# Kernel optimization log

Hardware: AMD Instinct MI355X
Metric: run time of the kernel (lower is better)

Reference implementation:

```python
import jax, jax.numpy as jnp
import numpy as np

BN_EPS = 1e-5

def conv1x1(x, w, b):
    # x: [N,C,T,V], w: [O,C], b: [O]
    return jnp.einsum('nctv,oc->notv', x, w) + b[None, :, None, None]

def conv9(x, w, b):
    # (9,1) temporal conv, padding (4,0). x: [N,C,T,V], w: [O,C,9], b: [O]
    out = jax.lax.conv_general_dilated(
        x, w[:, :, :, None], window_strides=(1, 1), padding=((4, 4), (0, 0)),
        dimension_numbers=('NCHW', 'OIHW', 'NCHW'))
    return out + b[None, :, None, None]

def attn_adj(f1, f2):
    # f1,f2: [N,inter,T,V] -> softmax over rows (axis -2) of [N,V,V]
    N, ic, T, V = f1.shape
    a1 = jnp.transpose(f1, (0, 3, 1, 2)).reshape(N, V, ic * T)  # permute(0,3,1,2).view
    a2 = f2.reshape(N, ic * T, V)
    scores = jnp.einsum('nvk,nkw->nvw', a1, a2) / (ic * T)
    return jax.nn.softmax(scores, axis=-2)


def setup_inputs() -> dict:
    key = jax.random.key(0)
    ks = jax.random.split(key, 16)
    N, C, T, V, S, IC = 16, 256, 64, 25, 3, 64
    s = lambda k, shape, sc=0.05: jax.random.normal(k, shape, dtype=jnp.float32) * sc
    return {
        'x': jax.random.normal(ks[0], (N, C, T, V), dtype=jnp.float32),
        'A': jax.random.uniform(ks[1], (S, V, V), dtype=jnp.float32),
        'PA': s(ks[2], (S, V, V), 1e-3),
        'wa': s(ks[3], (S, IC, C)), 'ba': jnp.zeros((S, IC), jnp.float32),
        'wb': s(ks[4], (S, IC, C)), 'bb': jnp.zeros((S, IC), jnp.float32),
        'wT1': s(ks[5], (S, IC, C, 9)), 'bT1': jnp.zeros((S, IC), jnp.float32),
        'wT2': s(ks[6], (S, IC, C, 9)), 'bT2': jnp.zeros((S, IC), jnp.float32),
        'wST11': s(ks[7], (S, IC, C, 9)), 'bST11': jnp.zeros((S, IC), jnp.float32),
        'wST12': s(ks[8], (S, IC, C, 9)), 'bST12': jnp.zeros((S, IC), jnp.float32),
        'wd': s(ks[9], (S, C, C)), 'bd': jnp.zeros((S, C), jnp.float32),
        'gamma': jnp.ones((C,), jnp.float32), 'beta': jnp.zeros((C,), jnp.float32),
        'bn_mean': jnp.zeros((C,), jnp.float32), 'bn_var': jnp.ones((C,), jnp.float32),
    }


def reference(x, A, PA, wa, ba, wb, bb, wT1, bT1, wT2, bT2,
              wST11, bST11, wST12, bST12, wd, bd, gamma, beta, bn_mean, bn_var):
    N, C, T, V = x.shape
    I = jnp.eye(V, dtype=x.dtype)
    # Chebyshev-like static graph transforms (computed once in __init__ in torch)
    A_ch4s = jax.nn.softmax((8 * A**4 - 4 * A**2 - 4 * A + I) / V, axis=-2)
    A_ch3 = 4 * A**2 - A - 2 * I
    A_all = A_ch3 + A_ch4s + PA  # [3,V,V]

    xf = x.reshape(N, C * T, V)
    y = 0.0
    for i in range(3):
        A1 = attn_adj(conv1x1(x, wa[i], ba[i]), conv1x1(x, wb[i], bb[i]))
        AT = attn_adj(conv9(x, wT1[i], bT1[i]), conv9(x, wT2[i], bT2[i]))
        # ModuleList append quirk: even i -> 1x1 conv (center tap), odd i -> (9,1) conv
        if i % 2 == 0:
            s1 = conv1x1(x, wST11[i, :, :, 4], bST11[i])
            s2 = conv1x1(x, wST12[i, :, :, 4], bST12[i])
        else:
            s1 = conv9(x, wST11[i], bST11[i])
            s2 = conv9(x, wST12[i], bST12[i])
        AST = attn_adj(s1, s2)
        Ai = A_all[i] + A1 + AT + AST  # [N,V,V]
        z = jnp.einsum('nkv,nvw->nkw', xf, Ai).reshape(N, C, T, V)
        y = y + conv1x1(z, wd[i], bd[i])

    yb = (y - bn_mean[None, :, None, None]) * (gamma[None, :, None, None]
         / jnp.sqrt(bn_var[None, :, None, None] + BN_EPS)) + beta[None, :, None, None]
    return jax.nn.relu(yb + x)  # down is identity (in_channels == out_channels)
```

## Files before the change

### kernel.cpp

```cpp
#include <hip/hip_runtime.h>
#include <hip/hip_bf16.h>

#define NN 16
#define CC 256
#define TT 64
#define VV 25
#define ICC 64
#define TV 1600
#define CTV 409600
#define NICTV 1638400

typedef __bf16 v8bf __attribute__((ext_vector_type(8)));
typedef __bf16 v4bf __attribute__((ext_vector_type(4)));
typedef float f32x16 __attribute__((ext_vector_type(16)));

struct ConvPairs {
  const __bf16* wA[5];
  const __bf16* wB[5];
  const float*  bA[5];
  const float*  bB[5];
};

__global__ __launch_bounds__(256) void prep_k(
    const float* __restrict__ x, __bf16* __restrict__ xt,
    const float* __restrict__ wT1, const float* __restrict__ wT2,
    const float* __restrict__ wST11, const float* __restrict__ wST12,
    __bf16* __restrict__ wT1p, __bf16* __restrict__ wT2p,
    __bf16* __restrict__ wS1p, __bf16* __restrict__ wS2p,
    const float* __restrict__ wa, const float* __restrict__ wb,
    __bf16* __restrict__ wabp, __bf16* __restrict__ wScp,
    const float* __restrict__ wd, __bf16* __restrict__ wdb,
    const float* __restrict__ A, const float* __restrict__ PA,
    float* __restrict__ Aall){
  __shared__ __align__(16) float smf[64*65];
  __bf16* smb = (__bf16*)smf;
  int b = blockIdx.x;
  int tid = threadIdx.x;
  if (b < 64){
    int t = b >> 3, ch = (b >> 1) & 3, o2 = b & 1;
    const float* src; __bf16* dst;
    if (t < 3)      { src = wT1  + (size_t)t*147456;     dst = wT1p + (size_t)t*147456; }
    else if (t < 6) { src = wT2  + (size_t)(t-3)*147456; dst = wT2p + (size_t)(t-3)*147456; }
    else if (t == 6){ src = wST11 + 147456;              dst = wS1p; }
    else            { src = wST12 + 147456;              dst = wS2p; }
    const float* in = src + (size_t)(o2*32)*2304 + ch*576;
    for (int i = tid; i < 32*576; i += 256){
      int row = i / 576, cc = i % 576;
      smb[i] = (__bf16)in[(size_t)row*2304 + cc];
    }
    __syncthreads();
    for (int i = tid; i < 18432; i += 256){
      int e = i & 7, l = (i >> 3) & 63, ks = (i >> 9) & 3, tap = i >> 11;
      int ol = l & 31, hh = l >> 5;
      int cl = ks*16 + hh*8 + e;
      dst[(size_t)((((ch*9 + tap)*4 + ks)*2 + o2)*512) + l*8 + e]
          = smb[ol*576 + cl*9 + tap];
    }
  } else if (b < 74){
    int u = b - 64;
    for (int it = 0; it < 8; ++it){
      int idx = tid + it*256;
      int l = idx & 63, o2 = (idx >> 6) & 1, ks = (idx >> 7) & 7, ch = idx >> 10;
      int o = o2*32 + (l & 31), hh = l >> 5;
      int cb = ch*128 + ks*16 + hh*8;
      __bf16 v[8];
      if (u < 6){
        const float* w = (u < 3) ? (wa + (size_t)u*16384) : (wb + (size_t)(u-3)*16384);
        const float* p = w + (size_t)o*256 + cb;
        #pragma unroll
        for (int e = 0; e < 8; ++e) v[e] = (__bf16)p[e];
      } else {
        int i9 = ((u == 6) || (u == 8)) ? 0 : 2;
        const float* w = ((u < 8) ? wST11 : wST12) + (size_t)i9*147456;
        const float* p = w + ((size_t)o*256 + cb)*9 + 4;
        #pragma unroll
        for (int e = 0; e < 8; ++e) v[e] = (__bf16)p[(size_t)e*9];
      }
      __bf16* dst = (u < 6) ? (wabp + (size_t)u*16384) : (wScp + (size_t)(u-6)*16384);
      #pragma unroll
      for (int e = 0; e < 8; ++e) dst[(size_t)idx*8 + e] = v[e];
    }
  } else if (b < 842){
    int i = (b-74)*256 + tid;
    if (i < 196608) wdb[i] = (__bf16)wd[i];
  } else if (b == 842){
    int t = tid;
    if (t < 75){
      int s = t / 25, w = t % 25;
      float a[25], m[25];
      float mx = -3.4e38f;
      for (int v = 0; v < 25; ++v){
        float av = A[(s*25 + v)*25 + w];
        a[v] = av;
        float d = (v == w) ? 1.f : 0.f;
        float mm = (8.f*av*av*av*av - 4.f*av*av - 4.f*av + d) * 0.04f;
        m[v] = mm;
        mx = fmaxf(mx, mm);
      }
      float sum = 0.f;
      for (int v = 0; v < 25; ++v){ float e = __expf(m[v]-mx); m[v] = e; sum += e; }
      float inv = 1.f/sum;
      for (int v = 0; v < 25; ++v){
        float av = a[v];
        float d = (v == w) ? 1.f : 0.f;
        Aall[(s*25+v)*25 + w] = m[v]*inv + 4.f*av*av - av - 2.f*d + PA[(s*25+v)*25+w];
      }
    }
  } else {
    int idx = b - 843;
    int p0 = (idx % 25)*64, c0 = ((idx/25) & 3)*64, n = idx/100;
    for (int i = tid; i < 4096; i += 256){
      int cc = i >> 6, pp = i & 63;
      smf[cc*65+pp] = x[(size_t)n*CTV + (size_t)(c0+cc)*TV + p0 + pp];
    }
    __syncthreads();
    for (int i = tid; i < 4096; i += 256){
      int pp = i >> 6, cc = i & 63;
      xt[((size_t)n*TV + p0+pp)*256 + c0+cc] = (__bf16)smf[cc*65+pp];
    }
  }
}

template<int NTAPS, int CW>
__global__ __launch_bounds__(256, 2) void conv7_k(const __bf16* __restrict__ xt,
    ConvPairs cp, __bf16* __restrict__ fbuf){
  extern __shared__ __bf16 sm[];
  constexpr int HALO  = (NTAPS==9) ? 100 : 0;
  constexpr int NROWS = 256 + 2*HALO;
  constexpr int GPR   = CW/8;
  constexpr int NCH   = 256/CW;
  constexpr int KS    = CW/16;
  constexpr int NSTEP = NTAPS*KS;
  int p0 = blockIdx.x*256;
  int n  = blockIdx.y;
  int pr = blockIdx.z;
  int tid = threadIdx.x;
  int lane = tid & 63;
  int wq = tid >> 6;
  int h = lane >> 5, l31 = lane & 31;
  const __bf16* wpA = cp.wA[pr] + lane*8;
  const __bf16* wpB = cp.wB[pr] + lane*8;
  const __bf16* xtn = xt + (size_t)n*CTV;

  f32x16 acc[4][2];
  #pragma unroll
  for (int a=0;a<4;++a)
    #pragma unroll
    for (int b=0;b<2;++b)
      #pragma unroll
      for (int r=0;r<16;++r) acc[a][b][r] = 0.f;

  int rowbase = wq*64 + l31;

  for (int ch=0; ch<NCH; ++ch){
    for (int s2 = tid; s2 < NROWS*GPR; s2 += 256){
      int row = s2 / GPR, g = s2 % GPR;
      int pg = p0 - HALO + row;
      uint4 val = make_uint4(0u,0u,0u,0u);
      if ((unsigned)pg < 1600u)
        val = *(const uint4*)(xtn + (size_t)pg*256 + ch*CW + g*8);
      int gs = (g + row) & (GPR-1);
      *(uint4*)(sm + row*CW + gs*8) = val;
    }
    __syncthreads();
    auto ldA = [&](int s, v8bf* aa){
      int tap = s / KS, ks = s % KS;
      size_t o = (size_t)((ch*NTAPS + tap)*KS + ks)*1024;
      aa[0] = *(const v8bf*)(wpA + o);
      aa[1] = *(const v8bf*)(wpA + o + 512);
      aa[2] = *(const v8bf*)(wpB + o);
      aa[3] = *(const v8bf*)(wpB + o + 512);
    };
    auto ldB = [&](int s, v8bf* bb){
      int tap = s / KS, ks = s % KS;
      int rowb = (NTAPS==9 ? tap*25 : 0) + rowbase;
      #pragma unroll
      for (int pq=0; pq<2; ++pq){
        int row = rowb + pq*32;
        int gs = ((ks*2 + h) + row) & (GPR-1);
        bb[pq] = *(const v8bf*)(sm + row*CW + gs*8);
      }
    };
    v8bf ar[2][4];
    ldA(0, ar[0]);
    ldA(1, ar[1]);
    v8bf bc[2], bn[2];
    ldB(0, bc);
    #pragma unroll
    for (int s=0; s<NSTEP; ++s){
      if (s+1 < NSTEP) ldB(s+1, bn);
      int cur = s & 1;
      v8bf A0 = ar[cur][0], A1 = ar[cur][1], A2 = ar[cur][2], A3 = ar[cur][3];
      if (s+2 < NSTEP) ldA(s+2, ar[cur]);
      #pragma unroll
      for (int pq=0; pq<2; ++pq){
        acc[0][pq] = __builtin_amdgcn_mfma_f32_32x32x16_bf16(A0, bc[pq], acc[0][pq], 0,0,0);
        acc[1][pq] = __builtin_amdgcn_mfma_f32_32x32x16_bf16(A1, bc[pq], acc[1][pq], 0,0,0);
        acc[2][pq] = __builtin_amdgcn_mfma_f32_32x32x16_bf16(A2, bc[pq], acc[2][pq], 0,0,0);
        acc[3][pq] = __builtin_amdgcn_mfma_f32_32x32x16_bf16(A3, bc[pq], acc[3][pq], 0,0,0);
      }
      bc[0] = bn[0]; bc[1] = bn[1];
    }
    __syncthreads();
  }

  #pragma unroll
  for (int f=0; f<4; ++f){
    int which = f >> 1, o2 = f & 1;
    const float* bias = which ? cp.bB[pr] : cp.bA[pr];
    __bf16* outb = fbuf + (size_t)(pr*2 + which)*NICTV + (size_t)n*TV*64;
    #pragma unroll
    for (int pq=0; pq<2; ++pq){
      int p = p0 + wq*64 + pq*32 + l31;
      if (p >= 1600) continue;
      __bf16* orow = outb + (size_t)p*64;
      #pragma unroll
      for (int g=0; g<4; ++g){
        int og = o2*32 + 8*g + 4*h;
        v4bf pk;
        #pragma unroll
        for (int j=0;j<4;++j) pk[j] = (__bf16)(acc[f][pq][4*g+j] + bias[og+j]);
        *(v4bf*)(orow + og) = pk;
      }
    }
  }
}

__global__ __launch_bounds__(256, 2) void ugemm5_k(const __bf16* __restrict__ xt,
    const __bf16* __restrict__ wdb, __bf16* __restrict__ ubuf){
  extern __shared__ __bf16 sm[];
  int p0 = blockIdx.x*128;
  int n  = blockIdx.y;
  int br = blockIdx.z;
  int tid = threadIdx.x;
  int lane = tid & 63;
  int os = tid >> 6;
  int h = lane >> 5, l31 = lane & 31;
  const __bf16* xtn = xt + (size_t)n*CTV;

  f32x16 acc[2][4];
  #pragma unroll
  for (int a=0;a<2;++a)
    #pragma unroll
    for (int b=0;b<4;++b)
      #pragma unroll
      for (int r=0;r<16;++r) acc[a][b][r] = 0.f;

  for (int s2 = tid; s2 < 128*32; s2 += 256){
    int row = s2 >> 5, g = s2 & 31;
    int pg = p0 + row;
    uint4 val = make_uint4(0u,0u,0u,0u);
    if (pg < 1600)
      val = *(const uint4*)(xtn + (size_t)pg*256 + g*8);
    int gs = (g + row) & 31;
    *(uint4*)(sm + row*256 + gs*8) = val;
  }
  __syncthreads();

  const __bf16* wl = wdb + ((size_t)br*256 + os*64 + l31)*256 + h*8;
  auto ldA = [&](int ks, v8bf& A0, v8bf& A1){
    A0 = *(const v8bf*)(wl + ks*16);
    A1 = *(const v8bf*)(wl + (size_t)32*256 + ks*16);
  };
  auto ldB = [&](int ks, v8bf* bb){
    #pragma unroll
    for (int pq=0; pq<4; ++pq){
      int row = pq*32 + l31;
      int gs = ((ks*2 + h) + row) & 31;
      bb[pq] = *(const v8bf*)(sm + row*256 + gs*8);
    }
  };
  v8bf a0[4], a1[4];
  ldA(0, a0[0], a1[0]);
  ldA(1, a0[1], a1[1]);
  ldA(2, a0[2], a1[2]);
  ldA(3, a0[3], a1[3]);
  v8bf bc[4], bn[4];
  ldB(0, bc);
  #pragma unroll
  for (int ks=0; ks<16; ++ks){
    if (ks+1 < 16) ldB(ks+1, bn);
    int cur = ks & 3;
    v8bf A0 = a0[cur], A1 = a1[cur];
    if (ks+4 < 16) ldA(ks+4, a0[cur], a1[cur]);
    #pragma unroll
    for (int pq=0; pq<4; ++pq){
      acc[0][pq] = __builtin_amdgcn_mfma_f32_32x32x16_bf16(A0, bc[pq], acc[0][pq], 0,0,0);
      acc[1][pq] = __builtin_amdgcn_mfma_f32_32x32x16_bf16(A1, bc[pq], acc[1][pq], 0,0,0);
    }
    #pragma unroll
    for (int pq=0; pq<4; ++pq) bc[pq] = bn[pq];
  }

  #pragma unroll
  for (int pq=0; pq<4; ++pq){
    int p = p0 + pq*32 + l31;
    if (p >= 1600) continue;
    __bf16* out = ubuf + ((size_t)(br*NN + n)*TV + p)*256;
    #pragma unroll
    for (int oq=0; oq<2; ++oq){
      #pragma unroll
      for (int g=0; g<4; ++g){
        int og = os*64 + oq*32 + 8*g + 4*h;
        v4bf pk;
        #pragma unroll
        for (int j=0;j<4;++j) pk[j] = (__bf16)acc[oq][pq][4*g+j];
        *(v4bf*)(out + og) = pk;
      }
    }
  }
}

__global__ __launch_bounds__(256) void scores_m_k(const __bf16* __restrict__ fbuf,
                                                  float* __restrict__ part, int pairbase){
  int n = blockIdx.y, pr = blockIdx.z;
  int tid = threadIdx.x;
  int lane = tid & 63;
  int wave = tid >> 6;
  int chunk = blockIdx.x*4 + wave;
  int h = lane >> 5, l31 = lane & 31;
  const __bf16* f1 = fbuf + (size_t)(pr*2)*NICTV   + (size_t)n*TV*64;
  const __bf16* f2 = fbuf + (size_t)(pr*2+1)*NICTV + (size_t)n*TV*64;
  int t0 = chunk*4;

  f32x16 acc;
  #pragma unroll
  for (int r=0;r<16;++r) acc[r] = 0.f;

  auto off = [&](int s)->size_t{
    int t = t0 + (s>>2), og = s&3;
    return ((size_t)(t*25 + l31))*64 + og*16 + h*8;
  };
  v8bf A[2], B[2];
  { size_t o0 = off(0); A[0] = *(const v8bf*)(f1+o0); B[0] = *(const v8bf*)(f2+o0); }
  { size_t o1 = off(1); A[1] = *(const v8bf*)(f1+o1); B[1] = *(const v8bf*)(f2+o1); }
  #pragma unroll
  for (int s=0; s<16; ++s){
    int cur = s & 1;
    v8bf Ac = A[cur], Bc = B[cur];
    if (s+2 < 16){
      size_t o2 = off(s+2);
      A[cur] = *(const v8bf*)(f1+o2);
      B[cur] = *(const v8bf*)(f2+o2);
    }
    acc = __builtin_amdgcn_mfma_f32_32x32x16_bf16(Ac, Bc, acc, 0,0,0);
  }

  size_t tile = (((size_t)(pairbase+pr)*NN + n)*16 + chunk);
  float* pt = part + tile*1024;
  #pragma unroll
  for (int r=0; r<16; ++r){
    int row = (r&3) + 8*(r>>2) + 4*h;
    pt[row*32 + l31] = acc[r];
  }
}

__global__ __launch_bounds__(64) void reduce_all_k(const float* __restrict__ part,
    const float* __restrict__ Aall, float* __restrict__ Ai3){
  const int pairbr[9] = {0,1,2,0,2, 0,1,2,1};
  int n = blockIdx.x, w = blockIdx.y;
  int lane = threadIdx.x;
  float accbr[3] = {0.f, 0.f, 0.f};
  for (int pr=0; pr<9; ++pr){
    float s = 0.f;
    if (lane < 25){
      const float* pp = part + (((size_t)pr*NN + n)*16)*1024 + lane*32 + w;
      #pragma unroll
      for (int ch=0; ch<16; ++ch) s += pp[(size_t)ch*1024];
    }
    s *= (1.f/4096.f);
    float mval = (lane<25) ? s : -3.4e38f;
    #pragma unroll
    for (int d=32; d>0; d>>=1) mval = fmaxf(mval, __shfl_xor(mval, d));
    float e = (lane<25) ? __expf(s - mval) : 0.f;
    float sum = e;
    #pragma unroll
    for (int d=32; d>0; d>>=1) sum += __shfl_xor(sum, d);
    accbr[pairbr[pr]] += e / sum;
  }
  if (lane < 25){
    #pragma unroll
    for (int br=0; br<3; ++br)
      Ai3[((size_t)br*NN + n)*625 + lane*25 + w] =
        Aall[br*625 + lane*25 + w] + accbr[br];
  }
}

__global__ __launch_bounds__(256) void yep_k(const float* __restrict__ x,
    const float* __restrict__ Ai3, const __bf16* __restrict__ ubuf,
    const float* __restrict__ bd, const float* __restrict__ gamma,
    const float* __restrict__ beta, const float* __restrict__ bnm,
    const float* __restrict__ bnv, float* __restrict__ out){
  __shared__ float ais[3][25*28];
  int t = blockIdx.x, n = blockIdx.y, o = threadIdx.x;
  for (int l=o; l<2100; l+=256){
    int br = l/700, r = l%700;
    int v = r/28, w = r%28;
    ais[br][v*28+w] = (w<25) ? Ai3[((size_t)br*NN + n)*625 + v*25 + w] : 0.f;
  }
  __syncthreads();
  float y[28];
  #pragma unroll
  for (int w=0;w<28;++w) y[w]=0.f;
  for (int br=0; br<3; ++br){
    const __bf16* up = ubuf + ((size_t)(br*NN + n)*TV + t*25)*256 + o;
    float uv[25];
    #pragma unroll
    for (int v=0;v<25;++v) uv[v] = (float)up[(size_t)v*256];
    const float* ab = ais[br];
    for (int v=0; v<25; ++v){
      float u = uv[v];
      #pragma unroll
      for (int j=0; j<7; ++j){
        float4 a4 = *(const float4*)(ab + v*28 + 4*j);
        y[4*j+0] = fmaf(u, a4.x, y[4*j+0]);
        y[4*j+1] = fmaf(u, a4.y, y[4*j+1]);
        y[4*j+2] = fmaf(u, a4.z, y[4*j+2]);
        y[4*j+3] = fmaf(u, a4.w, y[4*j+3]);
      }
    }
  }
  float bsum = bd[o] + bd[256+o] + bd[512+o];
  float sc = gamma[o] * rsqrtf(bnv[o] + 1e-5f);
  float m  = bnm[o], be = beta[o];
  const float* xr = x + (size_t)n*CTV + (size_t)o*TV + t*25;
  float* orow = out + (size_t)n*CTV + (size_t)o*TV + t*25;
  #pragma unroll
  for (int w=0; w<25; ++w)
    orow[w] = fmaxf((y[w] + bsum - m)*sc + be + xr[w], 0.f);
}

extern "C" void kernel_launch(void* const* d_in, const int* in_sizes, int n_in,
                              void* d_out, int out_size, void* d_ws, size_t ws_size,
                              hipStream_t stream) {
  const float* x     = (const float*)d_in[0];
  const float* A     = (const float*)d_in[1];
  const float* PA    = (const float*)d_in[2];
  const float* wa    = (const float*)d_in[3];
  const float* ba    = (const float*)d_in[4];
  const float* wb    = (const float*)d_in[5];
  const float* bb    = (const float*)d_in[6];
  const float* wT1   = (const float*)d_in[7];
  const float* bT1   = (const float*)d_in[8];
  const float* wT2   = (const float*)d_in[9];
  const float* bT2   = (const float*)d_in[10];
  const float* wST11 = (const float*)d_in[11];
  const float* bST11 = (const float*)d_in[12];
  const float* wST12 = (const float*)d_in[13];
  const float* bST12 = (const float*)d_in[14];
  const float* wd    = (const float*)d_in[15];
  const float* bd    = (const float*)d_in[16];
  const float* gamma = (const float*)d_in[17];
  const float* beta  = (const float*)d_in[18];
  const float* bnm   = (const float*)d_in[19];
  const float* bnv   = (const float*)d_in[20];

  char* W = (char*)d_ws;
  float*  Aall = (float*)W;  W += 8192;
  float*  Ai3  = (float*)W;  W += 122880;
  __bf16* wabp = (__bf16*)W; W += 196608;
  __bf16* wScp = (__bf16*)W; W += 131072;
  __bf16* wT1p = (__bf16*)W; W += 884736;
  __bf16* wT2p = (__bf16*)W; W += 884736;
  __bf16* wS1p = (__bf16*)W; W += 294912;
  __bf16* wS2p = (__bf16*)W; W += 294912;
  __bf16* wdb  = (__bf16*)W; W += 393216;
  __bf16* xt   = (__bf16*)W; W += 13107200;
  char* R = W;               W += 39321600;
  float*  part = (float*)W;  W += 9437184;
  __bf16* fbuf = (__bf16*)R;
  __bf16* ubuf = (__bf16*)R;

  prep_k<<<2443, 256, 0, stream>>>(x, xt, wT1, wT2, wST11, wST12,
                                   wT1p, wT2p, wS1p, wS2p,
                                   wa, wb, wabp, wScp, wd, wdb, A, PA, Aall);

  {
    ConvPairs cp;
    for (int i=0;i<3;++i){
      cp.wA[i] = wabp + (size_t)i*16384;      cp.wB[i] = wabp + (size_t)(3+i)*16384;
      cp.bA[i] = ba + i*64;                   cp.bB[i] = bb + i*64;
    }
    int evens[2] = {0, 2};
    for (int j=0;j<2;++j){
      int i = evens[j];
      cp.wA[3+j] = wScp + (size_t)j*16384;    cp.wB[3+j] = wScp + (size_t)(2+j)*16384;
      cp.bA[3+j] = bST11 + i*64;              cp.bB[3+j] = bST12 + i*64;
    }
    conv7_k<1,128><<<dim3(7,16,5), 256, 256*128*2, stream>>>(xt, cp, fbuf);
    scores_m_k<<<dim3(4,16,5), 256, 0, stream>>>(fbuf, part, 0);
  }

  {
    ConvPairs cp;
    for (int i=0;i<3;++i){
      cp.wA[i] = wT1p + (size_t)i*147456;  cp.wB[i] = wT2p + (size_t)i*147456;
      cp.bA[i] = bT1 + i*64;               cp.bB[i] = bT2 + i*64;
    }
    cp.wA[3] = wS1p;  cp.wB[3] = wS2p;
    cp.bA[3] = bST11 + 64;  cp.bB[3] = bST12 + 64;
    cp.wA[4] = cp.wA[3]; cp.wB[4] = cp.wB[3]; cp.bA[4] = cp.bA[3]; cp.bB[4] = cp.bB[3];
    conv7_k<9,64><<<dim3(7,16,4), 256, 456*64*2, stream>>>(xt, cp, fbuf);
    scores_m_k<<<dim3(4,16,4), 256, 0, stream>>>(fbuf, part, 5);
  }

  ugemm5_k<<<dim3(13,16,3), 256, 128*256*2, stream>>>(xt, wdb, ubuf);
  reduce_all_k<<<dim3(16,25), 64, 0, stream>>>(part, Aall, Ai3);
  yep_k<<<dim3(64,16), 256, 0, stream>>>(x, Ai3, ubuf, bd, gamma, beta, bnm, bnv,
                                         (float*)d_out);
}
```

Measured before the change: 357.0 us.

## Double the conv block to 512 threads and prefetch the next channel chunk into registers

The conv kernel now runs 512 threads per block, each wave owning 32 positions instead of 64, which halves the accumulators per thread and targets higher occupancy (launch bounds 512,4). It issues global loads for the next channel chunk into registers while the current chunk's MFMAs run, then writes them to shared memory between barriers, so staging overlaps with compute. Weight and shared-memory fragment prefetch depth rises to four steps. The ugemm and scores kernels likewise get deeper register prefetch. The cost is more live registers per thread and an extra barrier per chunk.

```diff
diff --git a/kernel.cpp b/kernel.cpp
--- a/kernel.cpp
+++ b/kernel.cpp
@@ -122,7 +122,7 @@
 }
 
 template<int NTAPS, int CW>
-__global__ __launch_bounds__(256, 2) void conv7_k(const __bf16* __restrict__ xt,
+__global__ __launch_bounds__(512, 4) void conv8_k(const __bf16* __restrict__ xt,
     ConvPairs cp, __bf16* __restrict__ fbuf){
   extern __shared__ __bf16 sm[];
   constexpr int HALO  = (NTAPS==9) ? 100 : 0;
@@ -131,6 +131,8 @@
   constexpr int NCH   = 256/CW;
   constexpr int KS    = CW/16;
   constexpr int NSTEP = NTAPS*KS;
+  constexpr int NSL   = NROWS*GPR;
+  constexpr int NLD   = (NSL + 511)/512;
   int p0 = blockIdx.x*256;
   int n  = blockIdx.y;
   int pr = blockIdx.z;
@@ -142,84 +144,105 @@
   const __bf16* wpB = cp.wB[pr] + lane*8;
   const __bf16* xtn = xt + (size_t)n*CTV;
 
-  f32x16 acc[4][2];
+  f32x16 acc[4];
   #pragma unroll
   for (int a=0;a<4;++a)
     #pragma unroll
-    for (int b=0;b<2;++b)
-      #pragma unroll
-      for (int r=0;r<16;++r) acc[a][b][r] = 0.f;
-
-  int rowbase = wq*64 + l31;
+    for (int r=0;r<16;++r) acc[a][r] = 0.f;
+
+  int rowbase = wq*32 + l31;
+
+  uint4 sv[NLD];
+  auto stageIssue = [&](int ch){
+    #pragma unroll
+    for (int k=0; k<NLD; ++k){
+      int s2 = tid + k*512;
+      uint4 val = make_uint4(0u,0u,0u,0u);
+      if ((NSL % 512 == 0) || (s2 < NSL)){
+        int row = s2 / GPR, g = s2 % GPR;
+        int pg = p0 - HALO + row;
+        if ((unsigned)pg < 1600u)
+          val = *(const uint4*)(xtn + (size_t)pg*256 + ch*CW + g*8);
+      }
+      sv[k] = val;
+    }
+  };
+  auto stageWrite = [&](){
+    #pragma unroll
+    for (int k=0; k<NLD; ++k){
+      int s2 = tid + k*512;
+      if ((NSL % 512 == 0) || (s2 < NSL)){
+        int row = s2 / GPR, g = s2 % GPR;
+        int gs = (g + row) & (GPR-1);
+        *(uint4*)(sm + row*CW + gs*8) = sv[k];
+      }
+    }
+  };
+
+  auto ldA = [&](int ch, int s, v8bf* aa){
+    int tap = s / KS, ks = s % KS;
+    size_t o = (size_t)((ch*NTAPS + tap)*KS + ks)*1024;
+    aa[0] = *(const v8bf*)(wpA + o);
+    aa[1] = *(const v8bf*)(wpA + o + 512);
+    aa[2] = *(const v8bf*)(wpB + o);
+    aa[3] = *(const v8bf*)(wpB + o + 512);
+  };
+  auto ldB = [&](int s, v8bf& bb){
+    int tap = s / KS, ks = s % KS;
+    int row = (NTAPS==9 ? tap*25 : 0) + rowbase;
+    int gs = ((ks*2 + h) + row) & (GPR-1);
+    bb = *(const v8bf*)(sm + row*CW + gs*8);
+  };
+
+  v8bf ar[4][4];
+  v8bf br_[4];
+
+  #pragma unroll
+  for (int s=0;s<4;++s) ldA(0, s, ar[s]);
+  stageIssue(0);
+  stageWrite();
+  __syncthreads();
 
   for (int ch=0; ch<NCH; ++ch){
-    for (int s2 = tid; s2 < NROWS*GPR; s2 += 256){
-      int row = s2 / GPR, g = s2 % GPR;
-      int pg = p0 - HALO + row;
-      uint4 val = make_uint4(0u,0u,0u,0u);
-      if ((unsigned)pg < 1600u)
-        val = *(const uint4*)(xtn + (size_t)pg*256 + ch*CW + g*8);
-      int gs = (g + row) & (GPR-1);
-      *(uint4*)(sm + row*CW + gs*8) = val;
-    }
-    __syncthreads();
-    auto ldA = [&](int s, v8bf* aa){
-      int tap = s / KS, ks = s % KS;
-      size_t o = (size_t)((ch*NTAPS + tap)*KS + ks)*1024;
-      aa[0] = *(const v8bf*)(wpA + o);
-      aa[1] = *(const v8bf*)(wpA + o + 512);
-      aa[2] = *(const v8bf*)(wpB + o);
-      aa[3] = *(const v8bf*)(wpB + o + 512);
-    };
-    auto ldB = [&](int s, v8bf* bb){
-      int tap = s / KS, ks = s % KS;
-      int rowb = (NTAPS==9 ? tap*25 : 0) + rowbase;
-      #pragma unroll
-      for (int pq=0; pq<2; ++pq){
-        int row = rowb + pq*32;
-        int gs = ((ks*2 + h) + row) & (GPR-1);
-        bb[pq] = *(const v8bf*)(sm + row*CW + gs*8);
-      }
-    };
-    v8bf ar[2][4];
-    ldA(0, ar[0]);
-    ldA(1, ar[1]);
-    v8bf bc[2], bn[2];
-    ldB(0, bc);
+    if (ch+1 < NCH) stageIssue(ch+1);
+    ldB(0, br_[0]); ldB(1, br_[1]); ldB(2, br_[2]); ldB(3, br_[3]);
     #pragma unroll
     for (int s=0; s<NSTEP; ++s){
-      if (s+1 < NSTEP) ldB(s+1, bn);
-      int cur = s & 1;
-      v8bf A0 = ar[cur][0], A1 = ar[cur][1], A2 = ar[cur][2], A3 = ar[cur][3];
-      if (s+2 < NSTEP) ldA(s+2, ar[cur]);
-      #pragma unroll
-      for (int pq=0; pq<2; ++pq){
-        acc[0][pq] = __builtin_amdgcn_mfma_f32_32x32x16_bf16(A0, bc[pq], acc[0][pq], 0,0,0);
-        acc[1][pq] = __builtin_amdgcn_mfma_f32_32x32x16_bf16(A1, bc[pq], acc[1][pq], 0,0,0);
-        acc[2][pq] = __builtin_amdgcn_mfma_f32_32x32x16_bf16(A2, bc[pq], acc[2][pq], 0,0,0);
-        acc[3][pq] = __builtin_amdgcn_mfma_f32_32x32x16_bf16(A3, bc[pq], acc[3][pq], 0,0,0);
-      }
-      bc[0] = bn[0]; bc[1] = bn[1];
-    }
-    __syncthreads();
-  }
-
-  #pragma unroll
-  for (int f=0; f<4; ++f){
-    int which = f >> 1, o2 = f & 1;
-    const float* bias = which ? cp.bB[pr] : cp.bA[pr];
-    __bf16* outb = fbuf + (size_t)(pr*2 + which)*NICTV + (size_t)n*TV*64;
-    #pragma unroll
-    for (int pq=0; pq<2; ++pq){
-      int p = p0 + wq*64 + pq*32 + l31;
-      if (p >= 1600) continue;
-      __bf16* orow = outb + (size_t)p*64;
+      int c = s & 3;
+      v8bf B0 = br_[c];
+      v8bf A0 = ar[c][0], A1 = ar[c][1], A2 = ar[c][2], A3 = ar[c][3];
+      if (s+4 < NSTEP){
+        ldB(s+4, br_[c]);
+        ldA(ch, s+4, ar[c]);
+      } else if (ch+1 < NCH){
+        ldA(ch+1, s+4-NSTEP, ar[c]);
+      }
+      acc[0] = __builtin_amdgcn_mfma_f32_32x32x16_bf16(A0, B0, acc[0], 0,0,0);
+      acc[1] = __builtin_amdgcn_mfma_f32_32x32x16_bf16(A1, B0, acc[1], 0,0,0);
+      acc[2] = __builtin_amdgcn_mfma_f32_32x32x16_bf16(A2, B0, acc[2], 0,0,0);
+      acc[3] = __builtin_amdgcn_mfma_f32_32x32x16_bf16(A3, B0, acc[3], 0,0,0);
+    }
+    if (ch+1 < NCH){
+      __syncthreads();
+      stageWrite();
+      __syncthreads();
+    }
+  }
+
+  int p = p0 + wq*32 + l31;
+  if (p < 1600){
+    #pragma unroll
+    for (int f=0; f<4; ++f){
+      int which = f >> 1, o2 = f & 1;
+      const float* bias = which ? cp.bB[pr] : cp.bA[pr];
+      __bf16* orow = fbuf + (size_t)(pr*2 + which)*NICTV + (size_t)n*TV*64
+                   + (size_t)p*64;
       #pragma unroll
       for (int g=0; g<4; ++g){
         int og = o2*32 + 8*g + 4*h;
         v4bf pk;
         #pragma unroll
-        for (int j=0;j<4;++j) pk[j] = (__bf16)(acc[f][pq][4*g+j] + bias[og+j]);
+        for (int j=0;j<4;++j) pk[j] = (__bf16)(acc[f][4*g+j] + bias[og+j]);
         *(v4bf*)(orow + og) = pk;
       }
     }
@@ -275,21 +298,24 @@
   ldA(1, a0[1], a1[1]);
   ldA(2, a0[2], a1[2]);
   ldA(3, a0[3], a1[3]);
-  v8bf bc[4], bn[4];
-  ldB(0, bc);
+  v8bf bR[2][4];
+  ldB(0, bR[0]);
+  ldB(1, bR[1]);
   #pragma unroll
   for (int ks=0; ks<16; ++ks){
-    if (ks+1 < 16) ldB(ks+1, bn);
-    int cur = ks & 3;
+    int c2 = ks & 1, cur = ks & 3;
+    v8bf B0 = bR[c2][0], B1 = bR[c2][1], B2 = bR[c2][2], B3 = bR[c2][3];
     v8bf A0 = a0[cur], A1 = a1[cur];
+    if (ks+2 < 16) ldB(ks+2, bR[c2]);
     if (ks+4 < 16) ldA(ks+4, a0[cur], a1[cur]);
-    #pragma unroll
-    for (int pq=0; pq<4; ++pq){
-      acc[0][pq] = __builtin_amdgcn_mfma_f32_32x32x16_bf16(A0, bc[pq], acc[0][pq], 0,0,0);
-      acc[1][pq] = __builtin_amdgcn_mfma_f32_32x32x16_bf16(A1, bc[pq], acc[1][pq], 0,0,0);
-    }
-    #pragma unroll
-    for (int pq=0; pq<4; ++pq) bc[pq] = bn[pq];
+    acc[0][0] = __builtin_amdgcn_mfma_f32_32x32x16_bf16(A0, B0, acc[0][0], 0,0,0);
+    acc[1][0] = __builtin_amdgcn_mfma_f32_32x32x16_bf16(A1, B0, acc[1][0], 0,0,0);
+    acc[0][1] = __builtin_amdgcn_mfma_f32_32x32x16_bf16(A0, B1, acc[0][1], 0,0,0);
+    acc[1][1] = __builtin_amdgcn_mfma_f32_32x32x16_bf16(A1, B1, acc[1][1], 0,0,0);
+    acc[0][2] = __builtin_amdgcn_mfma_f32_32x32x16_bf16(A0, B2, acc[0][2], 0,0,0);
+    acc[1][2] = __builtin_amdgcn_mfma_f32_32x32x16_bf16(A1, B2, acc[1][2], 0,0,0);
+    acc[0][3] = __builtin_amdgcn_mfma_f32_32x32x16_bf16(A0, B3, acc[0][3], 0,0,0);
+    acc[1][3] = __builtin_amdgcn_mfma_f32_32x32x16_bf16(A1, B3, acc[1][3], 0,0,0);
   }
 
   #pragma unroll
@@ -331,15 +357,18 @@
     int t = t0 + (s>>2), og = s&3;
     return ((size_t)(t*25 + l31))*64 + og*16 + h*8;
   };
-  v8bf A[2], B[2];
-  { size_t o0 = off(0); A[0] = *(const v8bf*)(f1+o0); B[0] = *(const v8bf*)(f2+o0); }
-  { size_t o1 = off(1); A[1] = *(const v8bf*)(f1+o1); B[1] = *(const v8bf*)(f2+o1); }
+  v8bf A[4], B[4];
+  #pragma unroll
+  for (int i=0; i<4; ++i){
+    size_t o = off(i);
+    A[i] = *(const v8bf*)(f1+o); B[i] = *(const v8bf*)(f2+o);
+  }
   #pragma unroll
   for (int s=0; s<16; ++s){
-    int cur = s & 1;
+    int cur = s & 3;
     v8bf Ac = A[cur], Bc = B[cur];
-    if (s+2 < 16){
-      size_t o2 = off(s+2);
+    if (s+4 < 16){
+      size_t o2 = off(s+4);
       A[cur] = *(const v8bf*)(f1+o2);
       B[cur] = *(const v8bf*)(f2+o2);
     }
@@ -487,7 +516,7 @@
       cp.wA[3+j] = wScp + (size_t)j*16384;    cp.wB[3+j] = wScp + (size_t)(2+j)*16384;
       cp.bA[3+j] = bST11 + i*64;              cp.bB[3+j] = bST12 + i*64;
     }
-    conv7_k<1,128><<<dim3(7,16,5), 256, 256*128*2, stream>>>(xt, cp, fbuf);
+    conv8_k<1,128><<<dim3(7,16,5), 512, 256*128*2, stream>>>(xt, cp, fbuf);
     scores_m_k<<<dim3(4,16,5), 256, 0, stream>>>(fbuf, part, 0);
   }
 
@@ -500,7 +529,7 @@
     cp.wA[3] = wS1p;  cp.wB[3] = wS2p;
     cp.bA[3] = bST11 + 64;  cp.bB[3] = bST12 + 64;
     cp.wA[4] = cp.wA[3]; cp.wB[4] = cp.wB[3]; cp.bA[4] = cp.bA[3]; cp.bB[4] = cp.bB[3];
-    conv7_k<9,64><<<dim3(7,16,4), 256, 456*64*2, stream>>>(xt, cp, fbuf);
+    conv8_k<9,64><<<dim3(7,16,4), 512, 456*64*2, stream>>>(xt, cp, fbuf);
     scores_m_k<<<dim3(4,16,4), 256, 0, stream>>>(fbuf, part, 5);
   }
 
```

Result: slower. 513.5 us (+43.8%).
